# Kernel tuning notes

Hardware: AMD Instinct MI355X
Metric: run time of the kernel (lower is better)

The kernel has to match this reference:

```python
import jax, jax.numpy as jnp
import numpy as np

C = 768
H = 12
N = 257
B = 64
HID = 4 * C
EPS = 1e-5
SCALE = (C // H) ** -0.5


def layer_norm(x, g, b):
    m = x.mean(-1, keepdims=True)
    v = ((x - m) ** 2).mean(-1, keepdims=True)
    return (x - m) * jax.lax.rsqrt(v + EPS) * g + b


def qkv_split(x, qkv_w):
    # x: [B,N,C]; qkv_w: [3C,C] (torch Linear layout)
    qkv = jnp.einsum('bnc,oc->bno', x, qkv_w)  # [B,N,3C]
    qkv = qkv.reshape(x.shape[0], x.shape[1], 3, H, C // H)
    qkv = jnp.transpose(qkv, (2, 0, 3, 1, 4))  # [3,B,H,N,hd]
    return qkv[0], qkv[1], qkv[2]


def self_attn(x, qkv_w, proj_w, proj_b):
    q, k, v = qkv_split(x, qkv_w)
    attn = jax.nn.softmax(jnp.einsum('bhnd,bhmd->bhnm', q, k) * SCALE, axis=-1)
    o = jnp.einsum('bhnm,bhmd->bhnd', attn, v)
    o = jnp.transpose(o, (0, 2, 1, 3)).reshape(x.shape)
    return jnp.einsum('bnc,oc->bno', o, proj_w) + proj_b


def cross_attn(x, y, qkv_w, proj_w, proj_b):
    qx, _, _ = qkv_split(x, qkv_w)
    _, ky, vy = qkv_split(y, qkv_w)
    attn = jax.nn.softmax(jnp.einsum('bhnd,bhmd->bhnm', qx, ky) * SCALE, axis=-1)
    o = jnp.einsum('bhnm,bhmd->bhnd', attn, vy)
    o = jnp.transpose(o, (0, 2, 1, 3)).reshape(x.shape)
    return jnp.einsum('bnc,oc->bno', o, proj_w) + proj_b, attn.sum(1)  # [B,N,N]


def mlp(x, w1, b1, w2, b2):
    h = jax.nn.gelu(jnp.einsum('bnc,hc->bnh', x, w1) + b1, approximate=False)
    return jnp.einsum('bnh,ch->bnc', h, w2) + b2


def arf(x):
    tmp = (jnp.exp(x) - jnp.exp(-x)) / (jnp.exp(x) + jnp.exp(-x - 4.0))
    return jnp.where(tmp < 0, jnp.zeros_like(x), tmp)


def setup_inputs() -> dict:
    key = jax.random.key(0)
    ks = jax.random.split(key, 16)
    s = 0.02
    return {
        'src': jax.random.normal(ks[0], (B, N, C), jnp.float32),
        'tgt': jax.random.normal(ks[1], (B, N, C), jnp.float32),
        'sattn_qkv_w': jax.random.normal(ks[2], (3 * C, C), jnp.float32) * s,
        'sattn_proj_w': jax.random.normal(ks[3], (C, C), jnp.float32) * s,
        'sattn_proj_b': jnp.zeros((C,), jnp.float32),
        'cattn_qkv_w': jax.random.normal(ks[4], (3 * C, C), jnp.float32) * s,
        'cattn_proj_w': jax.random.normal(ks[5], (C, C), jnp.float32) * s,
        'cattn_proj_b': jnp.zeros((C,), jnp.float32),
        'norm1_g': jnp.ones((C,), jnp.float32),
        'norm1_b': jnp.zeros((C,), jnp.float32),
        'norm2_g': jnp.ones((C,), jnp.float32),
        'norm2_b': jnp.zeros((C,), jnp.float32),
        'fc1_w': jax.random.normal(ks[6], (HID, C), jnp.float32) * s,
        'fc1_b': jnp.zeros((HID,), jnp.float32),
        'fc2_w': jax.random.normal(ks[7], (C, HID), jnp.float32) * s,
        'fc2_b': jnp.zeros((C,), jnp.float32),
        'sa_weight': jnp.ones((1, 1, C), jnp.float32),
        'pos_embed': jax.random.normal(ks[8], (1, N, C), jnp.float32) * s,
    }


def reference(src, tgt, sattn_qkv_w, sattn_proj_w, sattn_proj_b,
              cattn_qkv_w, cattn_proj_w, cattn_proj_b,
              norm1_g, norm1_b, norm2_g, norm2_b,
              fc1_w, fc1_b, fc2_w, fc2_b, sa_weight, pos_embed):
    src = src + pos_embed
    srct = self_attn(layer_norm(src, norm1_g, norm1_b), sattn_qkv_w, sattn_proj_w, sattn_proj_b)
    tgtt = self_attn(layer_norm(tgt, norm1_g, norm1_b), sattn_qkv_w, sattn_proj_w, sattn_proj_b)
    src = src + srct
    tgt = tgt + tgtt
    src = src + mlp(layer_norm(srct, norm2_g, norm2_b), fc1_w, fc1_b, fc2_w, fc2_b)
    tgt = tgt + mlp(layer_norm(tgtt, norm2_g, norm2_b), fc1_w, fc1_b, fc2_w, fc2_b)
    srct, attn_src = cross_attn(layer_norm(src, norm1_g, norm1_b),
                                layer_norm(tgt, norm1_g, norm1_b),
                                cattn_qkv_w, cattn_proj_w, cattn_proj_b)
    srct = arf(srct)
    src = src + srct
    src = src + mlp(layer_norm(srct, norm2_g, norm2_b), fc1_w, fc1_b, fc2_w, fc2_b)
    attm_out = attn_src[:, 1:, 1:]
    # heat gate (no grad through attn_src here)
    heat = jax.lax.stop_gradient(attn_src)
    heat = heat.mean(1).reshape(attn_src.shape[0], N, 1)  # [B,N,1]
    gate = jax.nn.sigmoid(heat)
    tgt = tgt + tgt * sa_weight * gate
    return src, tgt, attm_out
```

## Files before the change

kernel.cpp:

```cpp
#include <hip/hip_runtime.h>

#define N_SEQ  257
#define BATCH  64
#define CDIM   768
#define HEADS  12
#define HDIM   64
#define HIDDEN 3072
#define MROWS  (BATCH * N_SEQ)

typedef unsigned short u16;
typedef unsigned int   u32;
typedef __bf16 bf16x8 __attribute__((ext_vector_type(8)));
typedef float  f32x4  __attribute__((ext_vector_type(4)));

__device__ __forceinline__ float b2f(u16 u) { u32 x = ((u32)u) << 16; return __uint_as_float(x); }
__device__ __forceinline__ u16   f2b(float f) {
    u32 x = __float_as_uint(f);
    u32 r = (x + 0x7fffu + ((x >> 16) & 1u)) >> 16;
    return (u16)r;
}
__device__ __forceinline__ float ldf(const float x) { return x; }
__device__ __forceinline__ float ldf(const u16 x)   { return b2f(x); }

__device__ __forceinline__ float geluf(float x) { return 0.5f * x * (1.f + erff(x * 0.70710678118654752f)); }
__device__ __forceinline__ float arff(float x) {
    if (x <= 0.f) return 0.f;
    float a = expf(-2.f * x);
    float c = expf(-2.f * x - 4.f);
    return (1.f - a) / (1.f + c);
}

template<bool MAXOP>
__device__ __forceinline__ float block_red(float v, float* scratch, int tid) {
#pragma unroll
    for (int off = 32; off > 0; off >>= 1) {
        float o = __shfl_down(v, off, 64);
        v = MAXOP ? fmaxf(v, o) : v + o;
    }
    if ((tid & 63) == 0) scratch[tid >> 6] = v;
    __syncthreads();
    float r = MAXOP ? fmaxf(fmaxf(scratch[0], scratch[1]), fmaxf(scratch[2], scratch[3]))
                    : (scratch[0] + scratch[1]) + (scratch[2] + scratch[3]);
    __syncthreads();
    return r;
}

__global__ void detect_kernel(const u16* __restrict__ g1, u32* __restrict__ flag)
{
    if (threadIdx.x == 0 && blockIdx.x == 0) *flag = (g1[0] == 0x3F80u) ? 1u : 0u;
}

__global__ __launch_bounds__(256)
void conv_kernel(const void* __restrict__ s, u16* __restrict__ d, int n,
                 const u32* __restrict__ flag)
{
    const int i = blockIdx.x * 256 + threadIdx.x;
    if (i >= n) return;
    if (*flag) d[i] = ((const u16*)s)[i];
    else       d[i] = f2b(((const float*)s)[i]);
}

#define LDSW 40

template<int EP>
__global__ __launch_bounds__(256)
void gemm_kernel(const u16* __restrict__ A, const u16* __restrict__ W,
                 const u16* __restrict__ bias, u16* __restrict__ Co,
                 float* __restrict__ resid, int M, int Ncols, int K)
{
    __shared__ __align__(16) u16 sA[128 * LDSW];
    __shared__ __align__(16) u16 sB[128 * LDSW];
    const int tid  = threadIdx.x;
    const int bm0  = blockIdx.y * 128;
    const int n0   = blockIdx.x * 128;
    const int lane = tid & 63, wave = tid >> 6;
    const int wm = (wave >> 1) << 6;
    const int wn = (wave & 1) << 6;
    const int r16 = lane & 15, quad = lane >> 4;

    f32x4 acc[4][4] = {};

    for (int k0 = 0; k0 < K; k0 += 32) {
        __syncthreads();
#pragma unroll
        for (int it = 0; it < 2; ++it) {
            int c2  = tid + (it << 8);
            int row = c2 >> 2;
            int col = (c2 & 3) << 3;
            int gm  = bm0 + row; if (gm >= M) gm = M - 1;
            *reinterpret_cast<uint4*>(&sA[row * LDSW + col]) =
                *reinterpret_cast<const uint4*>(A + (size_t)gm * K + k0 + col);
            *reinterpret_cast<uint4*>(&sB[row * LDSW + col]) =
                *reinterpret_cast<const uint4*>(W + (size_t)(n0 + row) * K + k0 + col);
        }
        __syncthreads();

        bf16x8 af[4], bfr[4];
#pragma unroll
        for (int i = 0; i < 4; ++i) {
            af[i]  = *reinterpret_cast<const bf16x8*>(&sA[(wm + i * 16 + r16) * LDSW + quad * 8]);
            bfr[i] = *reinterpret_cast<const bf16x8*>(&sB[(wn + i * 16 + r16) * LDSW + quad * 8]);
        }
#pragma unroll
        for (int i = 0; i < 4; ++i)
#pragma unroll
            for (int j = 0; j < 4; ++j)
                acc[i][j] = __builtin_amdgcn_mfma_f32_16x16x32_bf16(af[i], bfr[j], acc[i][j], 0, 0, 0);
    }

#pragma unroll
    for (int i = 0; i < 4; ++i) {
#pragma unroll
        for (int j = 0; j < 4; ++j) {
            const int gn = n0 + wn + j * 16 + r16;
            const float bv = bias ? b2f(bias[gn]) : 0.f;
#pragma unroll
            for (int r = 0; r < 4; ++r) {
                const int gm = bm0 + wm + i * 16 + quad * 4 + r;
                if (gm < M) {
                    float v = acc[i][j][r] + bv;
                    const size_t oidx = (size_t)gm * Ncols + gn;
                    if (EP == 1) v = geluf(v);
                    if (EP == 3) v = arff(v);
                    if (EP == 0 || EP == 1) Co[oidx] = f2b(v);
                    if (EP == 2 || EP == 3) { Co[oidx] = f2b(v); resid[oidx] += v; }
                    if (EP == 4) resid[oidx] += v;
                }
            }
        }
    }
}

template<typename T>
__global__ __launch_bounds__(256)
void ln_kernel(const T* __restrict__ x, const u16* __restrict__ g,
               const u16* __restrict__ be, u16* __restrict__ y)
{
    __shared__ float scratch[4];
    const int row = blockIdx.x, tid = threadIdx.x;
    const size_t base = (size_t)row * CDIM;
    float v[3];
#pragma unroll
    for (int i = 0; i < 3; ++i) v[i] = ldf(x[base + tid + i * 256]);
    float mean = block_red<false>(v[0] + v[1] + v[2], scratch, tid) * (1.f / 768.f);
    float d0 = v[0] - mean, d1 = v[1] - mean, d2 = v[2] - mean;
    float var = block_red<false>(d0 * d0 + d1 * d1 + d2 * d2, scratch, tid) * (1.f / 768.f);
    float rstd = rsqrtf(var + 1e-5f);
#pragma unroll
    for (int i = 0; i < 3; ++i) {
        int c = tid + i * 256;
        y[base + c] = f2b((v[i] - mean) * rstd * b2f(g[c]) + b2f(be[c]));
    }
}

__global__ __launch_bounds__(256, 4)
void attn_flash_kernel(const u16* __restrict__ Q, int qs,
                       const u16* __restrict__ Kp, int ks,
                       const u16* __restrict__ Vp, int vs,
                       u16* __restrict__ O, float* __restrict__ asum)
{
    __shared__ __align__(16) u16 Vt[2][64 * 64];
    __shared__ __align__(16) u16 Ps[64 * 72];
    const int tid = threadIdx.x;
    const int n0 = blockIdx.x * 64;
    const int h  = blockIdx.y, b = blockIdx.z;
    const int lane = tid & 63, w = tid >> 6;
    const int r16 = lane & 15, quad = lane >> 4;

    int qrow = n0 + w * 16 + r16; if (qrow > 256) qrow = 256;
    const u16* qp = Q + (size_t)(b * N_SEQ + qrow) * qs + h * HDIM + quad * 8;
    const bf16x8 af0 = *reinterpret_cast<const bf16x8*>(qp);
    const bf16x8 af1 = *reinterpret_cast<const bf16x8*>(qp + 32);

    auto stageV = [&](int kt, int buf) {
#pragma unroll
        for (int it = 0; it < 2; ++it) {
            int id  = tid + (it << 8);
            int key = id & 63;
            int dc  = ((id >> 6) & 7) << 3;
            int gm  = kt * 64 + key; if (gm > 256) gm = 256;
            uint4 v4 = *reinterpret_cast<const uint4*>(Vp + (size_t)(b * N_SEQ + gm) * vs + h * HDIM + dc);
            const u16* vv = reinterpret_cast<const u16*>(&v4);
#pragma unroll
            for (int j = 0; j < 8; ++j) {
                int d = dc + j;
                Vt[buf][d * 64 + (key ^ ((d & 7) << 3))] = vv[j];
            }
        }
    };

    f32x4 O4[4];
#pragma unroll
    for (int s = 0; s < 4; ++s) O4[s] = (f32x4){0.f, 0.f, 0.f, 0.f};
    float m_[4] = { -3.0e38f, -3.0e38f, -3.0e38f, -3.0e38f };
    float l_[4] = { 0.f, 0.f, 0.f, 0.f };

    stageV(0, 0);
    __syncthreads();

    for (int kt = 0; kt < 5; ++kt) {
        if (kt < 4) stageV(kt + 1, (kt + 1) & 1);

        f32x4 s4[4];
#pragma unroll
        for (int s = 0; s < 4; ++s) s4[s] = (f32x4){0.f, 0.f, 0.f, 0.f};
#pragma unroll
        for (int s = 0; s < 4; ++s) {
            int krow = kt * 64 + s * 16 + r16; if (krow > 256) krow = 256;
            const u16* kp = Kp + (size_t)(b * N_SEQ + krow) * ks + h * HDIM + quad * 8;
            bf16x8 b0 = *reinterpret_cast<const bf16x8*>(kp);
            bf16x8 b1 = *reinterpret_cast<const bf16x8*>(kp + 32);
            s4[s] = __builtin_amdgcn_mfma_f32_16x16x32_bf16(af0, b0, s4[s], 0, 0, 0);
            s4[s] = __builtin_amdgcn_mfma_f32_16x16x32_bf16(af1, b1, s4[s], 0, 0, 0);
        }

#pragma unroll
        for (int s = 0; s < 4; ++s)
#pragma unroll
            for (int r = 0; r < 4; ++r) {
                float v = s4[s][r] * 0.125f;
                if (kt == 4 && (s * 16 + r16) >= 1) v = -3.0e38f;
                s4[s][r] = v;
            }

#pragma unroll
        for (int r = 0; r < 4; ++r) {
            float tmax = fmaxf(fmaxf(s4[0][r], s4[1][r]), fmaxf(s4[2][r], s4[3][r]));
#pragma unroll
            for (int msk = 1; msk < 16; msk <<= 1) tmax = fmaxf(tmax, __shfl_xor(tmax, msk, 64));
            float mn = fmaxf(m_[r], tmax);
            float corr = __expf(m_[r] - mn);
            m_[r] = mn;
            float rs = 0.f;
#pragma unroll
            for (int s = 0; s < 4; ++s) {
                float p = __expf(s4[s][r] - mn);
                s4[s][r] = p; rs += p;
            }
#pragma unroll
            for (int msk = 1; msk < 16; msk <<= 1) rs += __shfl_xor(rs, msk, 64);
            l_[r] = l_[r] * corr + rs;
#pragma unroll
            for (int s = 0; s < 4; ++s) O4[s][r] *= corr;
        }

#pragma unroll
        for (int ts = 0; ts < 4; ++ts)
#pragma unroll
            for (int r = 0; r < 4; ++r)
                Ps[(w * 16 + quad * 4 + r) * 72 + ts * 16 + r16] = f2b(s4[ts][r]);
        bf16x8 p0 = *reinterpret_cast<const bf16x8*>(&Ps[(w * 16 + r16) * 72 + quad * 8]);
        bf16x8 p1 = *reinterpret_cast<const bf16x8*>(&Ps[(w * 16 + r16) * 72 + 32 + quad * 8]);
#pragma unroll
        for (int s = 0; s < 4; ++s) {
            const int d0 = s * 16 + r16;
            const int sw = (d0 & 7) << 3;
            bf16x8 v0 = *reinterpret_cast<const bf16x8*>(&Vt[kt & 1][d0 * 64 + ((quad * 8) ^ sw)]);
            bf16x8 v1 = *reinterpret_cast<const bf16x8*>(&Vt[kt & 1][d0 * 64 + ((32 + quad * 8) ^ sw)]);
            O4[s] = __builtin_amdgcn_mfma_f32_16x16x32_bf16(p0, v0, O4[s], 0, 0, 0);
            O4[s] = __builtin_amdgcn_mfma_f32_16x16x32_bf16(p1, v1, O4[s], 0, 0, 0);
        }

        __syncthreads();
    }

    float inv[4];
#pragma unroll
    for (int r = 0; r < 4; ++r) inv[r] = 1.f / l_[r];

#pragma unroll
    for (int s = 0; s < 4; ++s) {
#pragma unroll
        for (int r = 0; r < 4; ++r) {
            const int n = n0 + w * 16 + quad * 4 + r;
            if (n < N_SEQ)
                O[(size_t)(b * N_SEQ + n) * CDIM + h * HDIM + s * 16 + r16] = f2b(O4[s][r] * inv[r]);
        }
    }

    if (asum) {
        for (int kt = 0; kt < 5; ++kt) {
            f32x4 s4[4];
#pragma unroll
            for (int s = 0; s < 4; ++s) s4[s] = (f32x4){0.f, 0.f, 0.f, 0.f};
#pragma unroll
            for (int s = 0; s < 4; ++s) {
                int krow = kt * 64 + s * 16 + r16; if (krow > 256) krow = 256;
                const u16* kp = Kp + (size_t)(b * N_SEQ + krow) * ks + h * HDIM + quad * 8;
                bf16x8 b0 = *reinterpret_cast<const bf16x8*>(kp);
                bf16x8 b1 = *reinterpret_cast<const bf16x8*>(kp + 32);
                s4[s] = __builtin_amdgcn_mfma_f32_16x16x32_bf16(af0, b0, s4[s], 0, 0, 0);
                s4[s] = __builtin_amdgcn_mfma_f32_16x16x32_bf16(af1, b1, s4[s], 0, 0, 0);
            }
#pragma unroll
            for (int s = 0; s < 4; ++s)
#pragma unroll
                for (int r = 0; r < 4; ++r) {
                    const int key = kt * 64 + s * 16 + r16;
                    const int n = n0 + w * 16 + quad * 4 + r;
                    if (key < N_SEQ && n < N_SEQ) {
                        float p = __expf(s4[s][r] * 0.125f - m_[r]) * inv[r];
                        atomicAdd(&asum[((size_t)b * N_SEQ + n) * N_SEQ + key], p);
                    }
                }
        }
    }
}

__global__ __launch_bounds__(256)
void init_kernel(const void* __restrict__ src, const void* __restrict__ tgt,
                 const void* __restrict__ pos, float* __restrict__ sa,
                 float* __restrict__ ta, const u32* __restrict__ flag)
{
    const u32 i = blockIdx.x * 256 + threadIdx.x;
    const u32 p = i % (u32)(N_SEQ * CDIM);
    float sv, tv, pv;
    if (*flag) {
        sv = b2f(((const u16*)src)[i]); tv = b2f(((const u16*)tgt)[i]); pv = b2f(((const u16*)pos)[p]);
    } else {
        sv = ((const float*)src)[i];    tv = ((const float*)tgt)[i];    pv = ((const float*)pos)[p];
    }
    sa[i] = sv + pv;
    ta[i] = tv;
}

__global__ __launch_bounds__(256)
void zero_kernel(float* __restrict__ p, int n)
{
    const int i = blockIdx.x * 256 + threadIdx.x;
    if (i < n) p[i] = 0.f;
}

__global__ __launch_bounds__(256)
void gate_kernel(const float* __restrict__ asum, float* __restrict__ gate)
{
    const int b = blockIdx.x;
    for (int m = threadIdx.x; m < N_SEQ; m += 256) {
        float s = 0.f;
        for (int q = 0; q < N_SEQ; ++q)
            s += asum[((size_t)b * N_SEQ + q) * N_SEQ + m];
        s *= (1.f / 257.f);
        gate[b * N_SEQ + m] = 1.f / (1.f + expf(-s));
    }
}

__global__ __launch_bounds__(256)
void final_kernel(const float* __restrict__ sa, const float* __restrict__ ta,
                  const u16* __restrict__ saw, const float* __restrict__ gate,
                  void* __restrict__ osrc_v, const u32* __restrict__ flag)
{
    const u32 i = blockIdx.x * 256 + threadIdx.x;
    const int c  = i % CDIM;
    const int bn = i / CDIM;
    const float so = sa[i];
    const float to = ta[i] * (1.f + b2f(saw[c]) * gate[bn]);
    const size_t BNC = (size_t)MROWS * CDIM;
    if (*flag) {
        u16* o = (u16*)osrc_v;
        o[i] = f2b(so); o[BNC + i] = f2b(to);
    } else {
        float* o = (float*)osrc_v;
        o[i] = so; o[BNC + i] = to;
    }
}

__global__ __launch_bounds__(256)
void attm_kernel(const float* __restrict__ asum, void* __restrict__ out_v,
                 const u32* __restrict__ flag)
{
    const u32 i = blockIdx.x * 256 + threadIdx.x;
    const int b = i >> 16;
    const int r = (i >> 8) & 255;
    const int c = i & 255;
    const float v = asum[((size_t)b * N_SEQ + (r + 1)) * N_SEQ + (c + 1)];
    const size_t off = 2 * (size_t)MROWS * CDIM;
    if (*flag) ((u16*)out_v)[off + i] = f2b(v);
    else       ((float*)out_v)[off + i] = v;
}

extern "C" void kernel_launch(void* const* d_in, const int* in_sizes, int n_in,
                              void* d_out, int out_size, void* d_ws, size_t ws_size,
                              hipStream_t stream)
{
    const void* src    = d_in[0];
    const void* tgt    = d_in[1];
    const void* pos    = d_in[17];

    const int M = MROWS;
    const size_t BNC = (size_t)M * CDIM;

    float* SA   = (float*)d_ws;
    float* TA   = SA + BNC;
    u16*   Cb   = (u16*)(TA + BNC);
    u16*   Db   = Cb + BNC;
    u16*   Eb   = Db + BNC;
    float* ASUM = (float*)(Eb + 4 * BNC);
    float* GATE = ASUM + (size_t)BATCH * N_SEQ * N_SEQ;
    u16*   WB   = (u16*)(GATE + (size_t)BATCH * N_SEQ);
    u16* w_sqkv   = WB;
    u16* w_sproj  = w_sqkv  + 1769472;
    u16* w_sprojb = w_sproj + 589824;
    u16* w_cqkv   = w_sprojb + 768;
    u16* w_cproj  = w_cqkv  + 1769472;
    u16* w_cprojb = w_cproj + 589824;
    u16* w_g1     = w_cprojb + 768;
    u16* w_b1     = w_g1 + 768;
    u16* w_g2     = w_b1 + 768;
    u16* w_b2     = w_g2 + 768;
    u16* w_fc1    = w_b2 + 768;
    u16* w_fc1b   = w_fc1 + 2359296;
    u16* w_fc2    = w_fc1b + 3072;
    u16* w_fc2b   = w_fc2 + 2359296;
    u16* w_saw    = w_fc2b + 768;
    u32* FLAG     = (u32*)(w_saw + 768);
    if (ws_size < (size_t)((char*)(FLAG + 4) - (char*)d_ws)) return;

    const dim3 blk(256, 1, 1);
    const int gM = (M + 127) / 128;
    const dim3 agrid(5, HEADS, BATCH);

    detect_kernel<<<dim3(1), dim3(64), 0, stream>>>((const u16*)d_in[8], FLAG);

    auto conv = [&](int idx, u16* dst, int n) {
        conv_kernel<<<dim3((n + 255) / 256), blk, 0, stream>>>(d_in[idx], dst, n, FLAG);
    };
    conv(2,  w_sqkv,   1769472);
    conv(3,  w_sproj,  589824);
    conv(4,  w_sprojb, 768);
    conv(5,  w_cqkv,   1769472);
    conv(6,  w_cproj,  589824);
    conv(7,  w_cprojb, 768);
    conv(8,  w_g1,     768);
    conv(9,  w_b1,     768);
    conv(10, w_g2,     768);
    conv(11, w_b2,     768);
    conv(12, w_fc1,    2359296);
    conv(13, w_fc1b,   3072);
    conv(14, w_fc2,    2359296);
    conv(15, w_fc2b,   768);
    conv(16, w_saw,    768);

    init_kernel<<<dim3((u32)(BNC / 256)), blk, 0, stream>>>(src, tgt, pos, SA, TA, FLAG);

    ln_kernel<float><<<dim3(M), blk, 0, stream>>>(SA, w_g1, w_b1, Db);
    gemm_kernel<0><<<dim3(2304 / 128, gM), blk, 0, stream>>>(Db, w_sqkv, nullptr, Eb, nullptr, M, 2304, CDIM);
    attn_flash_kernel<<<agrid, blk, 0, stream>>>(Eb, 2304, Eb + 768, 2304, Eb + 1536, 2304, Db, nullptr);
    gemm_kernel<2><<<dim3(6, gM), blk, 0, stream>>>(Db, w_sproj, w_sprojb, Cb, SA, M, CDIM, CDIM);
    ln_kernel<u16><<<dim3(M), blk, 0, stream>>>(Cb, w_g2, w_b2, Db);
    gemm_kernel<1><<<dim3(HIDDEN / 128, gM), blk, 0, stream>>>(Db, w_fc1, w_fc1b, Eb, nullptr, M, HIDDEN, CDIM);
    gemm_kernel<4><<<dim3(6, gM), blk, 0, stream>>>(Eb, w_fc2, w_fc2b, nullptr, SA, M, CDIM, HIDDEN);

    ln_kernel<float><<<dim3(M), blk, 0, stream>>>(TA, w_g1, w_b1, Db);
    gemm_kernel<0><<<dim3(2304 / 128, gM), blk, 0, stream>>>(Db, w_sqkv, nullptr, Eb, nullptr, M, 2304, CDIM);
    attn_flash_kernel<<<agrid, blk, 0, stream>>>(Eb, 2304, Eb + 768, 2304, Eb + 1536, 2304, Db, nullptr);
    gemm_kernel<2><<<dim3(6, gM), blk, 0, stream>>>(Db, w_sproj, w_sprojb, Cb, TA, M, CDIM, CDIM);
    ln_kernel<u16><<<dim3(M), blk, 0, stream>>>(Cb, w_g2, w_b2, Db);
    gemm_kernel<1><<<dim3(HIDDEN / 128, gM), blk, 0, stream>>>(Db, w_fc1, w_fc1b, Eb, nullptr, M, HIDDEN, CDIM);
    gemm_kernel<4><<<dim3(6, gM), blk, 0, stream>>>(Eb, w_fc2, w_fc2b, nullptr, TA, M, CDIM, HIDDEN);

    u16* EKV = Eb + BNC;
    ln_kernel<float><<<dim3(M), blk, 0, stream>>>(SA, w_g1, w_b1, Db);
    gemm_kernel<0><<<dim3(6, gM), blk, 0, stream>>>(Db, w_cqkv, nullptr, Eb, nullptr, M, CDIM, CDIM);
    ln_kernel<float><<<dim3(M), blk, 0, stream>>>(TA, w_g1, w_b1, Db);
    gemm_kernel<0><<<dim3(12, gM), blk, 0, stream>>>(Db, w_cqkv + 768 * 768, nullptr, EKV, nullptr, M, 1536, CDIM);
    const int asum_n = BATCH * N_SEQ * N_SEQ;
    zero_kernel<<<dim3((asum_n + 255) / 256), blk, 0, stream>>>(ASUM, asum_n);
    attn_flash_kernel<<<agrid, blk, 0, stream>>>(Eb, 768, EKV, 1536, EKV + 768, 1536, Db, ASUM);
    gemm_kernel<3><<<dim3(6, gM), blk, 0, stream>>>(Db, w_cproj, w_cprojb, Cb, SA, M, CDIM, CDIM);
    ln_kernel<u16><<<dim3(M), blk, 0, stream>>>(Cb, w_g2, w_b2, Db);
    gemm_kernel<1><<<dim3(HIDDEN / 128, gM), blk, 0, stream>>>(Db, w_fc1, w_fc1b, Eb, nullptr, M, HIDDEN, CDIM);
    gemm_kernel<4><<<dim3(6, gM), blk, 0, stream>>>(Eb, w_fc2, w_fc2b, nullptr, SA, M, CDIM, HIDDEN);

    gate_kernel<<<dim3(BATCH), blk, 0, stream>>>(ASUM, GATE);
    final_kernel<<<dim3((u32)(BNC / 256)), blk, 0, stream>>>(SA, TA, w_saw, GATE, d_out, FLAG);
    attm_kernel<<<dim3(BATCH * 256 * 256 / 256), blk, 0, stream>>>(ASUM, d_out, FLAG);
}
```

Baseline: 2.692 ms.

## Replace atomic head-sum of attention probs with dedicated per-batch reduction kernel

The cross-attention kernel now only stores each row's softmax max and inverse normaliser. A new kernel recomputes the QK scores for every head and sums the probabilities in registers per (batch, query tile), then writes each output entry once. This removes the zeroing pass and roughly 12 atomic adds per output element, at the cost of a second QK^T pass and a small grid (5x64 blocks) holding 20 accumulators per thread.

```diff
diff --git a/kernel.cpp b/kernel.cpp
--- a/kernel.cpp
+++ b/kernel.cpp
@@ -157,7 +157,8 @@
 void attn_flash_kernel(const u16* __restrict__ Q, int qs,
                        const u16* __restrict__ Kp, int ks,
                        const u16* __restrict__ Vp, int vs,
-                       u16* __restrict__ O, float* __restrict__ asum)
+                       u16* __restrict__ O,
+                       float* __restrict__ Mg, float* __restrict__ Ig)
 {
     __shared__ __align__(16) u16 Vt[2][64 * 64];
     __shared__ __align__(16) u16 Ps[64 * 72];
@@ -268,6 +269,17 @@
 #pragma unroll
     for (int r = 0; r < 4; ++r) inv[r] = 1.f / l_[r];
 
+    if (Mg) {
+#pragma unroll
+        for (int r = 0; r < 4; ++r) {
+            const int n = n0 + w * 16 + quad * 4 + r;
+            if (r16 == 0 && n < N_SEQ) {
+                const size_t mi = (size_t)(b * HEADS + h) * N_SEQ + n;
+                Mg[mi] = m_[r]; Ig[mi] = inv[r];
+            }
+        }
+    }
+
 #pragma unroll
     for (int s = 0; s < 4; ++s) {
 #pragma unroll
@@ -277,34 +289,78 @@
                 O[(size_t)(b * N_SEQ + n) * CDIM + h * HDIM + s * 16 + r16] = f2b(O4[s][r] * inv[r]);
         }
     }
-
-    if (asum) {
-        for (int kt = 0; kt < 5; ++kt) {
-            f32x4 s4[4];
-#pragma unroll
-            for (int s = 0; s < 4; ++s) s4[s] = (f32x4){0.f, 0.f, 0.f, 0.f};
-#pragma unroll
-            for (int s = 0; s < 4; ++s) {
-                int krow = kt * 64 + s * 16 + r16; if (krow > 256) krow = 256;
-                const u16* kp = Kp + (size_t)(b * N_SEQ + krow) * ks + h * HDIM + quad * 8;
-                bf16x8 b0 = *reinterpret_cast<const bf16x8*>(kp);
-                bf16x8 b1 = *reinterpret_cast<const bf16x8*>(kp + 32);
-                s4[s] = __builtin_amdgcn_mfma_f32_16x16x32_bf16(af0, b0, s4[s], 0, 0, 0);
-                s4[s] = __builtin_amdgcn_mfma_f32_16x16x32_bf16(af1, b1, s4[s], 0, 0, 0);
-            }
-#pragma unroll
-            for (int s = 0; s < 4; ++s)
-#pragma unroll
-                for (int r = 0; r < 4; ++r) {
-                    const int key = kt * 64 + s * 16 + r16;
-                    const int n = n0 + w * 16 + quad * 4 + r;
-                    if (key < N_SEQ && n < N_SEQ) {
-                        float p = __expf(s4[s][r] * 0.125f - m_[r]) * inv[r];
-                        atomicAdd(&asum[((size_t)b * N_SEQ + n) * N_SEQ + key], p);
-                    }
-                }
-        }
-    }
+}
+
+__global__ __launch_bounds__(256, 2)
+void asum_kernel(const u16* __restrict__ Q, int qs,
+                 const u16* __restrict__ Kp, int ks,
+                 const float* __restrict__ Mg, const float* __restrict__ Ig,
+                 float* __restrict__ asum)
+{
+    const int tid = threadIdx.x;
+    const int n0 = blockIdx.x * 64;
+    const int b  = blockIdx.y;
+    const int lane = tid & 63, w = tid >> 6;
+    const int r16 = lane & 15, quad = lane >> 4;
+
+    f32x4 A00 = {0.f,0.f,0.f,0.f}, A01 = {0.f,0.f,0.f,0.f}, A02 = {0.f,0.f,0.f,0.f}, A03 = {0.f,0.f,0.f,0.f};
+    f32x4 A10 = {0.f,0.f,0.f,0.f}, A11 = {0.f,0.f,0.f,0.f}, A12 = {0.f,0.f,0.f,0.f}, A13 = {0.f,0.f,0.f,0.f};
+    f32x4 A20 = {0.f,0.f,0.f,0.f}, A21 = {0.f,0.f,0.f,0.f}, A22 = {0.f,0.f,0.f,0.f}, A23 = {0.f,0.f,0.f,0.f};
+    f32x4 A30 = {0.f,0.f,0.f,0.f}, A31 = {0.f,0.f,0.f,0.f}, A32 = {0.f,0.f,0.f,0.f}, A33 = {0.f,0.f,0.f,0.f};
+    f32x4 A40 = {0.f,0.f,0.f,0.f}, A41 = {0.f,0.f,0.f,0.f}, A42 = {0.f,0.f,0.f,0.f}, A43 = {0.f,0.f,0.f,0.f};
+
+    for (int h = 0; h < HEADS; ++h) {
+        int qrow = n0 + w * 16 + r16; if (qrow > 256) qrow = 256;
+        const u16* qp = Q + (size_t)(b * N_SEQ + qrow) * qs + h * HDIM + quad * 8;
+        const bf16x8 af0 = *reinterpret_cast<const bf16x8*>(qp);
+        const bf16x8 af1 = *reinterpret_cast<const bf16x8*>(qp + 32);
+
+        float mv[4], iv[4];
+#pragma unroll
+        for (int r = 0; r < 4; ++r) {
+            int n = n0 + w * 16 + quad * 4 + r; if (n > 256) n = 256;
+            const size_t mi = (size_t)(b * HEADS + h) * N_SEQ + n;
+            mv[r] = Mg[mi]; iv[r] = Ig[mi];
+        }
+
+#define ASUM_TS(KT, S, AV) { \
+        int krow = KT * 64 + S * 16 + r16; if (krow > 256) krow = 256; \
+        const u16* kp = Kp + (size_t)(b * N_SEQ + krow) * ks + h * HDIM + quad * 8; \
+        bf16x8 b0 = *reinterpret_cast<const bf16x8*>(kp); \
+        bf16x8 b1 = *reinterpret_cast<const bf16x8*>(kp + 32); \
+        f32x4 t = (f32x4){0.f, 0.f, 0.f, 0.f}; \
+        t = __builtin_amdgcn_mfma_f32_16x16x32_bf16(af0, b0, t, 0, 0, 0); \
+        t = __builtin_amdgcn_mfma_f32_16x16x32_bf16(af1, b1, t, 0, 0, 0); \
+        _Pragma("unroll") \
+        for (int r = 0; r < 4; ++r) { \
+            float p = __expf(t[r] * 0.125f - mv[r]) * iv[r]; \
+            if (KT == 4 && (S * 16 + r16) >= 1) p = 0.f; \
+            AV[r] += p; \
+        } }
+
+        ASUM_TS(0, 0, A00) ASUM_TS(0, 1, A01) ASUM_TS(0, 2, A02) ASUM_TS(0, 3, A03)
+        ASUM_TS(1, 0, A10) ASUM_TS(1, 1, A11) ASUM_TS(1, 2, A12) ASUM_TS(1, 3, A13)
+        ASUM_TS(2, 0, A20) ASUM_TS(2, 1, A21) ASUM_TS(2, 2, A22) ASUM_TS(2, 3, A23)
+        ASUM_TS(3, 0, A30) ASUM_TS(3, 1, A31) ASUM_TS(3, 2, A32) ASUM_TS(3, 3, A33)
+        ASUM_TS(4, 0, A40) ASUM_TS(4, 1, A41) ASUM_TS(4, 2, A42) ASUM_TS(4, 3, A43)
+#undef ASUM_TS
+    }
+
+#define ASUM_ST(KT, S, AV) { \
+    _Pragma("unroll") \
+    for (int r = 0; r < 4; ++r) { \
+        const int n = n0 + w * 16 + quad * 4 + r; \
+        const int key = KT * 64 + S * 16 + r16; \
+        if (n < N_SEQ && key < N_SEQ) \
+            asum[((size_t)b * N_SEQ + n) * N_SEQ + key] = AV[r]; \
+    } }
+
+    ASUM_ST(0, 0, A00) ASUM_ST(0, 1, A01) ASUM_ST(0, 2, A02) ASUM_ST(0, 3, A03)
+    ASUM_ST(1, 0, A10) ASUM_ST(1, 1, A11) ASUM_ST(1, 2, A12) ASUM_ST(1, 3, A13)
+    ASUM_ST(2, 0, A20) ASUM_ST(2, 1, A21) ASUM_ST(2, 2, A22) ASUM_ST(2, 3, A23)
+    ASUM_ST(3, 0, A30) ASUM_ST(3, 1, A31) ASUM_ST(3, 2, A32) ASUM_ST(3, 3, A33)
+    ASUM_ST(4, 0, A40) ASUM_ST(4, 1, A41) ASUM_ST(4, 2, A42) ASUM_ST(4, 3, A43)
+#undef ASUM_ST
 }
 
 __global__ __launch_bounds__(256)
@@ -322,13 +378,6 @@
     }
     sa[i] = sv + pv;
     ta[i] = tv;
-}
-
-__global__ __launch_bounds__(256)
-void zero_kernel(float* __restrict__ p, int n)
-{
-    const int i = blockIdx.x * 256 + threadIdx.x;
-    if (i < n) p[i] = 0.f;
 }
 
 __global__ __launch_bounds__(256)
@@ -413,7 +462,10 @@
     u16* w_fc2b   = w_fc2 + 2359296;
     u16* w_saw    = w_fc2b + 768;
     u32* FLAG     = (u32*)(w_saw + 768);
-    if (ws_size < (size_t)((char*)(FLAG + 4) - (char*)d_ws)) return;
+    const size_t NMI = (size_t)BATCH * HEADS * N_SEQ;
+    float* MG     = (float*)(FLAG + 4);
+    float* IG     = MG + NMI;
+    if (ws_size < (size_t)((char*)(IG + NMI) - (char*)d_ws)) return;
 
     const dim3 blk(256, 1, 1);
     const int gM = (M + 127) / 128;
@@ -444,7 +496,7 @@
 
     ln_kernel<float><<<dim3(M), blk, 0, stream>>>(SA, w_g1, w_b1, Db);
     gemm_kernel<0><<<dim3(2304 / 128, gM), blk, 0, stream>>>(Db, w_sqkv, nullptr, Eb, nullptr, M, 2304, CDIM);
-    attn_flash_kernel<<<agrid, blk, 0, stream>>>(Eb, 2304, Eb + 768, 2304, Eb + 1536, 2304, Db, nullptr);
+    attn_flash_kernel<<<agrid, blk, 0, stream>>>(Eb, 2304, Eb + 768, 2304, Eb + 1536, 2304, Db, nullptr, nullptr);
     gemm_kernel<2><<<dim3(6, gM), blk, 0, stream>>>(Db, w_sproj, w_sprojb, Cb, SA, M, CDIM, CDIM);
     ln_kernel<u16><<<dim3(M), blk, 0, stream>>>(Cb, w_g2, w_b2, Db);
     gemm_kernel<1><<<dim3(HIDDEN / 128, gM), blk, 0, stream>>>(Db, w_fc1, w_fc1b, Eb, nullptr, M, HIDDEN, CDIM);
@@ -452,7 +504,7 @@
 
     ln_kernel<float><<<dim3(M), blk, 0, stream>>>(TA, w_g1, w_b1, Db);
     gemm_kernel<0><<<dim3(2304 / 128, gM), blk, 0, stream>>>(Db, w_sqkv, nullptr, Eb, nullptr, M, 2304, CDIM);
-    attn_flash_kernel<<<agrid, blk, 0, stream>>>(Eb, 2304, Eb + 768, 2304, Eb + 1536, 2304, Db, nullptr);
+    attn_flash_kernel<<<agrid, blk, 0, stream>>>(Eb, 2304, Eb + 768, 2304, Eb + 1536, 2304, Db, nullptr, nullptr);
     gemm_kernel<2><<<dim3(6, gM), blk, 0, stream>>>(Db, w_sproj, w_sprojb, Cb, TA, M, CDIM, CDIM);
     ln_kernel<u16><<<dim3(M), blk, 0, stream>>>(Cb, w_g2, w_b2, Db);
     gemm_kernel<1><<<dim3(HIDDEN / 128, gM), blk, 0, stream>>>(Db, w_fc1, w_fc1b, Eb, nullptr, M, HIDDEN, CDIM);
@@ -463,9 +515,8 @@
     gemm_kernel<0><<<dim3(6, gM), blk, 0, stream>>>(Db, w_cqkv, nullptr, Eb, nullptr, M, CDIM, CDIM);
     ln_kernel<float><<<dim3(M), blk, 0, stream>>>(TA, w_g1, w_b1, Db);
     gemm_kernel<0><<<dim3(12, gM), blk, 0, stream>>>(Db, w_cqkv + 768 * 768, nullptr, EKV, nullptr, M, 1536, CDIM);
-    const int asum_n = BATCH * N_SEQ * N_SEQ;
-    zero_kernel<<<dim3((asum_n + 255) / 256), blk, 0, stream>>>(ASUM, asum_n);
-    attn_flash_kernel<<<agrid, blk, 0, stream>>>(Eb, 768, EKV, 1536, EKV + 768, 1536, Db, ASUM);
+    attn_flash_kernel<<<agrid, blk, 0, stream>>>(Eb, 768, EKV, 1536, EKV + 768, 1536, Db, MG, IG);
+    asum_kernel<<<dim3(5, BATCH), blk, 0, stream>>>(Eb, 768, EKV, 1536, MG, IG, ASUM);
     gemm_kernel<3><<<dim3(6, gM), blk, 0, stream>>>(Db, w_cproj, w_cprojb, Cb, SA, M, CDIM, CDIM);
     ln_kernel<u16><<<dim3(M), blk, 0, stream>>>(Cb, w_g2, w_b2, Db);
     gemm_kernel<1><<<dim3(HIDDEN / 128, gM), blk, 0, stream>>>(Db, w_fc1, w_fc1b, Eb, nullptr, M, HIDDEN, CDIM);
```

After: 2.523 ms. 6.3% less time.
